# Kernel optimization log

Measured on AMD Instinct MI355X. Metric: run time of the kernel, lower is better.

Reference implementation:

```python
import jax, jax.numpy as jnp
import numpy as np

FEATURES_DIM = 100000
NUM_FIELDS = 39
EMBED_DIM = 64
DIM_INT = (2, 3)
RANK = (32, 32)
BATCH = 8192


def setup_inputs() -> dict:
    key = jax.random.key(0)
    ks = jax.random.split(key, 6)
    x = jax.random.randint(ks[0], (BATCH, NUM_FIELDS), 0, FEATURES_DIM)
    embed_table = jax.random.normal(ks[1], (FEATURES_DIM, EMBED_DIM), dtype=jnp.float32) * 0.01
    linear_w = jax.random.normal(ks[2], (FEATURES_DIM, 1), dtype=jnp.float32) * 0.01
    linear_bias = jnp.zeros((1,), dtype=jnp.float32)
    # trunc_normal_(std=0.01) approximated by clipped normal
    W0 = jnp.clip(jax.random.normal(ks[3], (DIM_INT[0], RANK[0], NUM_FIELDS), dtype=jnp.float32) * 0.01, -0.02, 0.02)
    W1 = jnp.clip(jax.random.normal(ks[4], (DIM_INT[1], RANK[1], NUM_FIELDS), dtype=jnp.float32) * 0.01, -0.02, 0.02)
    return {"x": x, "embed_table": embed_table, "linear_w": linear_w,
            "linear_bias": linear_bias, "W0": W0, "W1": W1}


def _calc_cross(W, emb):
    # W: (l, j, k) = (dim_int, rank, num_fields); emb: (b, k, i) = (batch, fields, embed)
    # dot_products[b,i,j,l] = sum_k W[l,j,k] * emb[b,k,i]
    dp = jnp.einsum('ljk,bki->bijl', W, emb)          # (b, embed, rank, dim_int)
    prod_over_l = jnp.prod(dp, axis=3)                # (b, embed, rank)
    return jnp.sum(prod_over_l, axis=(1, 2))          # (b,)


def reference(x, embed_table, linear_w, linear_bias, W0, W1):
    emb = embed_table[x]                              # (b, fields, embed)
    lin = jnp.sum(linear_w[x], axis=1) + linear_bias  # (b, 1)
    ret = lin[:, 0] + _calc_cross(W0, emb) + _calc_cross(W1, emb)
    return ret                                        # (b,)
```

## Files before the change

### kernel.cpp

```cpp
#include <hip/hip_runtime.h>
#include <hip/hip_bf16.h>

#define BATCH    8192
#define NF       39
#define ED       64
#define RANK     32
#define SPW      2
#define KST      48
#define NFRAG    15

typedef _Float16 half8  __attribute__((ext_vector_type(8)));
typedef float    f32x16 __attribute__((ext_vector_type(16)));

__global__ void prep_w(const float* __restrict__ W0,
                       const float* __restrict__ W1,
                       half8* __restrict__ wsW) {
    int d = blockIdx.x * 256 + threadIdx.x;
    if (d >= NFRAG * 64) return;
    int fid  = d >> 6;
    int lane = d & 63;
    int l = fid / 3, kc = fid % 3;
    int j = lane & 31, kh = lane >> 5;
    const float* base = (l < 2) ? (W0 + (l * RANK + j) * NF)
                                : (W1 + ((l - 2) * RANK + j) * NF);
    half8 h;
#pragma unroll
    for (int e = 0; e < 8; ++e) {
        int k = kc * 16 + kh * 8 + e;
        h[e] = (k < NF) ? (_Float16)base[k] : (_Float16)0.0f;
    }
    wsW[d] = h;
}

__global__ __launch_bounds__(256, 3) void tfm_kernel(
    const int*   __restrict__ x,
    const float* __restrict__ embed,
    const float* __restrict__ linw,
    const float* __restrict__ lbias,
    const half8* __restrict__ wsW,
    float*       __restrict__ out)
{
    __shared__ __align__(16) _Float16 Es[4][SPW][ED][KST];

    const int t    = threadIdx.x;
    const int lane = t & 63;
    const int w    = t >> 6;
    const int s0   = (blockIdx.x * 4 + w) * SPW;

    const float bias = lbias[0];
    const int j  = lane & 31;
    const int kh = lane >> 5;

    int xv[SPW];
#pragma unroll
    for (int si = 0; si < SPW; ++si)
        xv[si] = (lane < NF) ? x[(s0 + si) * NF + lane] : 0;

    float lv[SPW];
#pragma unroll
    for (int si = 0; si < SPW; ++si)
        lv[si] = (lane < NF) ? linw[xv[si]] : 0.0f;

    half8 wf[5][3];
#pragma unroll
    for (int l = 0; l < 5; ++l)
#pragma unroll
        for (int kc = 0; kc < 3; ++kc)
            wf[l][kc] = wsW[(l * 3 + kc) * 64 + lane];

    float r[SPW][NF];
#pragma unroll
    for (int si = 0; si < SPW; ++si)
#pragma unroll
        for (int k = 0; k < NF; ++k) {
            int xi = __builtin_amdgcn_readlane(xv[si], k);
            r[si][k] = embed[(size_t)xi * ED + lane];
        }

#pragma unroll
    for (int si = 0; si < SPW; ++si)
#pragma unroll
        for (int c6 = 0; c6 < 6; ++c6) {
            half8 hh;
#pragma unroll
            for (int e = 0; e < 8; ++e) {
                int k = c6 * 8 + e;
                hh[e] = (k < NF) ? (_Float16)r[si][k] : (_Float16)0.0f;
            }
            *(half8*)&Es[w][si][lane][c6 * 8] = hh;
        }

#pragma unroll
    for (int si = 0; si < SPW; ++si) {
        float ssum = lv[si];

#pragma unroll
        for (int tile = 0; tile < 2; ++tile) {
            const int c = tile * 32 + j;
            half8 bf[3];
#pragma unroll
            for (int kc = 0; kc < 3; ++kc)
                bf[kc] = *(const half8*)&Es[w][si][c][kc * 16 + kh * 8];

            {
                f32x16 a0, a1;
#pragma unroll
                for (int e = 0; e < 16; ++e) { a0[e] = 0.0f; a1[e] = 0.0f; }
#pragma unroll
                for (int kc = 0; kc < 3; ++kc) {
                    a0 = __builtin_amdgcn_mfma_f32_32x32x16_f16(wf[0][kc], bf[kc], a0, 0, 0, 0);
                    a1 = __builtin_amdgcn_mfma_f32_32x32x16_f16(wf[1][kc], bf[kc], a1, 0, 0, 0);
                }
#pragma unroll
                for (int e = 0; e < 16; ++e) ssum += a0[e] * a1[e];
            }
            {
                f32x16 c0, c1, c2;
#pragma unroll
                for (int e = 0; e < 16; ++e) { c0[e] = 0.0f; c1[e] = 0.0f; c2[e] = 0.0f; }
#pragma unroll
                for (int kc = 0; kc < 3; ++kc) {
                    c0 = __builtin_amdgcn_mfma_f32_32x32x16_f16(wf[2][kc], bf[kc], c0, 0, 0, 0);
                    c1 = __builtin_amdgcn_mfma_f32_32x32x16_f16(wf[3][kc], bf[kc], c1, 0, 0, 0);
                    c2 = __builtin_amdgcn_mfma_f32_32x32x16_f16(wf[4][kc], bf[kc], c2, 0, 0, 0);
                }
#pragma unroll
                for (int e = 0; e < 16; ++e) ssum += c0[e] * c1[e] * c2[e];
            }
        }

#pragma unroll
        for (int off = 32; off > 0; off >>= 1) ssum += __shfl_down(ssum, off, 64);
        if (lane == 0) out[s0 + si] = ssum + bias;
    }
}

extern "C" void kernel_launch(void* const* d_in, const int* in_sizes, int n_in,
                              void* d_out, int out_size, void* d_ws, size_t ws_size,
                              hipStream_t stream) {
    const int*   x     = (const int*)  d_in[0];
    const float* embed = (const float*)d_in[1];
    const float* linw  = (const float*)d_in[2];
    const float* lbias = (const float*)d_in[3];
    const float* W0    = (const float*)d_in[4];
    const float* W1    = (const float*)d_in[5];
    float*       out   = (float*)d_out;
    half8*       wsW   = (half8*)d_ws;

    prep_w<<<(NFRAG * 64 + 255) / 256, 256, 0, stream>>>(W0, W1, wsW);
    tfm_kernel<<<BATCH / (4 * SPW), 256, 0, stream>>>(x, embed, linw, lbias, wsW, out);
}
```

Before: 99.20 us.

## Stage MFMA weight fragments in LDS and process one sample per wave

Moves the 15 weight fragments from per-lane registers into shared memory, loaded cooperatively once per block. Each wave now handles one sample instead of two, doubling the grid, and the LDS row stride grows from 48 to 72 halves, apparently to reduce bank conflicts. The aim is to cut VGPR pressure (no wf[5][3] array, half the gathered embedding registers) so more waves are resident and the random embedding gathers are better hidden. In exchange it adds a __syncthreads, an LDS read of the weights for every MFMA, and a per-block reload of the weights.

```diff
diff --git a/kernel.cpp b/kernel.cpp
--- a/kernel.cpp
+++ b/kernel.cpp
@@ -5,8 +5,7 @@
 #define NF       39
 #define ED       64
 #define RANK     32
-#define SPW      2
-#define KST      48
+#define KST      72
 #define NFRAG    15
 
 typedef _Float16 half8  __attribute__((ext_vector_type(8)));
@@ -40,99 +39,92 @@
     const half8* __restrict__ wsW,
     float*       __restrict__ out)
 {
-    __shared__ __align__(16) _Float16 Es[4][SPW][ED][KST];
+    __shared__ __align__(16) _Float16 Ws[NFRAG * 64 * 8];
+    __shared__ __align__(16) _Float16 Ef[4][ED][KST];
 
     const int t    = threadIdx.x;
     const int lane = t & 63;
     const int w    = t >> 6;
-    const int s0   = (blockIdx.x * 4 + w) * SPW;
+    const int s    = blockIdx.x * 4 + w;
 
-    const float bias = lbias[0];
     const int j  = lane & 31;
     const int kh = lane >> 5;
 
-    int xv[SPW];
+    const int xi_v = (lane < NF) ? x[s * NF + lane] : 0;
+    const float lv = (lane < NF) ? linw[xi_v] : 0.0f;
+
+    float r[NF];
 #pragma unroll
-    for (int si = 0; si < SPW; ++si)
-        xv[si] = (lane < NF) ? x[(s0 + si) * NF + lane] : 0;
+    for (int k = 0; k < NF; ++k) {
+        int xi = __builtin_amdgcn_readlane(xi_v, k);
+        r[k] = embed[(size_t)xi * ED + lane];
+    }
 
-    float lv[SPW];
+    {
+        const uint4* src = (const uint4*)wsW;
+        uint4*       dst = (uint4*)Ws;
 #pragma unroll
-    for (int si = 0; si < SPW; ++si)
-        lv[si] = (lane < NF) ? linw[xv[si]] : 0.0f;
+        for (int i = 0; i < NFRAG * 64 / 256; ++i)
+            dst[i * 256 + t] = src[i * 256 + t];
+        if (t < NFRAG * 64 - 768) dst[768 + t] = src[768 + t];
+    }
 
-    half8 wf[5][3];
+    const float bias = lbias[0];
+
 #pragma unroll
-    for (int l = 0; l < 5; ++l)
+    for (int c6 = 0; c6 < 6; ++c6) {
+        half8 hh;
+#pragma unroll
+        for (int e = 0; e < 8; ++e) {
+            int k = c6 * 8 + e;
+            hh[e] = (k < NF) ? (_Float16)r[k] : (_Float16)0.0f;
+        }
+        *(half8*)&Ef[w][lane][c6 * 8] = hh;
+    }
+
+    __syncthreads();
+
+    const half8* Wf = (const half8*)Ws;
+    float ssum = lv;
+
+#pragma unroll
+    for (int tile = 0; tile < 2; ++tile) {
+        const int c = tile * 32 + j;
+        half8 bf[3];
 #pragma unroll
         for (int kc = 0; kc < 3; ++kc)
-            wf[l][kc] = wsW[(l * 3 + kc) * 64 + lane];
+            bf[kc] = *(const half8*)&Ef[w][c][kc * 16 + kh * 8];
 
-    float r[SPW][NF];
+        {
+            f32x16 a0, a1;
 #pragma unroll
-    for (int si = 0; si < SPW; ++si)
+            for (int e = 0; e < 16; ++e) { a0[e] = 0.0f; a1[e] = 0.0f; }
 #pragma unroll
-        for (int k = 0; k < NF; ++k) {
-            int xi = __builtin_amdgcn_readlane(xv[si], k);
-            r[si][k] = embed[(size_t)xi * ED + lane];
+            for (int kc = 0; kc < 3; ++kc) {
+                a0 = __builtin_amdgcn_mfma_f32_32x32x16_f16(Wf[(0 * 3 + kc) * 64 + lane], bf[kc], a0, 0, 0, 0);
+                a1 = __builtin_amdgcn_mfma_f32_32x32x16_f16(Wf[(1 * 3 + kc) * 64 + lane], bf[kc], a1, 0, 0, 0);
+            }
+#pragma unroll
+            for (int e = 0; e < 16; ++e) ssum += a0[e] * a1[e];
         }
+        {
+            f32x16 c0, c1, c2;
+#pragma unroll
+            for (int e = 0; e < 16; ++e) { c0[e] = 0.0f; c1[e] = 0.0f; c2[e] = 0.0f; }
+#pragma unroll
+            for (int kc = 0; kc < 3; ++kc) {
+                c0 = __builtin_amdgcn_mfma_f32_32x32x16_f16(Wf[(2 * 3 + kc) * 64 + lane], bf[kc], c0, 0, 0, 0);
+                c1 = __builtin_amdgcn_mfma_f32_32x32x16_f16(Wf[(3 * 3 + kc) * 64 + lane], bf[kc], c1, 0, 0, 0);
+                c2 = __builtin_amdgcn_mfma_f32_32x32x16_f16(Wf[(4 * 3 + kc) * 64 + lane], bf[kc], c2, 0, 0, 0);
+            }
+#pragma unroll
+            for (int e = 0; e < 16; ++e) ssum += c0[e] * c1[e] * c2[e];
+        }
+    }
 
 #pragma unroll
-    for (int si = 0; si < SPW; ++si)
-#pragma unroll
-        for (int c6 = 0; c6 < 6; ++c6) {
-            half8 hh;
-#pragma unroll
-            for (int e = 0; e < 8; ++e) {
-                int k = c6 * 8 + e;
-                hh[e] = (k < NF) ? (_Float16)r[si][k] : (_Float16)0.0f;
-            }
-            *(half8*)&Es[w][si][lane][c6 * 8] = hh;
-        }
-
-#pragma unroll
-    for (int si = 0; si < SPW; ++si) {
-        float ssum = lv[si];
-
-#pragma unroll
-        for (int tile = 0; tile < 2; ++tile) {
-            const int c = tile * 32 + j;
-            half8 bf[3];
-#pragma unroll
-            for (int kc = 0; kc < 3; ++kc)
-                bf[kc] = *(const half8*)&Es[w][si][c][kc * 16 + kh * 8];
-
-            {
-                f32x16 a0, a1;
-#pragma unroll
-                for (int e = 0; e < 16; ++e) { a0[e] = 0.0f; a1[e] = 0.0f; }
-#pragma unroll
-                for (int kc = 0; kc < 3; ++kc) {
-                    a0 = __builtin_amdgcn_mfma_f32_32x32x16_f16(wf[0][kc], bf[kc], a0, 0, 0, 0);
-                    a1 = __builtin_amdgcn_mfma_f32_32x32x16_f16(wf[1][kc], bf[kc], a1, 0, 0, 0);
-                }
-#pragma unroll
-                for (int e = 0; e < 16; ++e) ssum += a0[e] * a1[e];
-            }
-            {
-                f32x16 c0, c1, c2;
-#pragma unroll
-                for (int e = 0; e < 16; ++e) { c0[e] = 0.0f; c1[e] = 0.0f; c2[e] = 0.0f; }
-#pragma unroll
-                for (int kc = 0; kc < 3; ++kc) {
-                    c0 = __builtin_amdgcn_mfma_f32_32x32x16_f16(wf[2][kc], bf[kc], c0, 0, 0, 0);
-                    c1 = __builtin_amdgcn_mfma_f32_32x32x16_f16(wf[3][kc], bf[kc], c1, 0, 0, 0);
-                    c2 = __builtin_amdgcn_mfma_f32_32x32x16_f16(wf[4][kc], bf[kc], c2, 0, 0, 0);
-                }
-#pragma unroll
-                for (int e = 0; e < 16; ++e) ssum += c0[e] * c1[e] * c2[e];
-            }
-        }
-
-#pragma unroll
-        for (int off = 32; off > 0; off >>= 1) ssum += __shfl_down(ssum, off, 64);
-        if (lane == 0) out[s0 + si] = ssum + bias;
-    }
+    for (int off = 32; off > 0; off >>= 1) ssum += __shfl_down(ssum, off, 64);
+    if (lane == 0) out[s] = ssum + bias;
 }
 
 extern "C" void kernel_launch(void* const* d_in, const int* in_sizes, int n_in,
@@ -148,5 +140,5 @@
     half8*       wsW   = (half8*)d_ws;
 
     prep_w<<<(NFRAG * 64 + 255) / 256, 256, 0, stream>>>(W0, W1, wsW);
-    tfm_kernel<<<BATCH / (4 * SPW), 256, 0, stream>>>(x, embed, linw, lbias, wsW, out);
+    tfm_kernel<<<BATCH / 4, 256, 0, stream>>>(x, embed, linw, lbias, wsW, out);
 }
```

Result: faster. 94.98 us (-4.3%).
